# Performance work log

Hardware: AMD Instinct MI355X
Metric: run time of the kernel (lower is better)

## Reference

```python
import jax, jax.numpy as jnp
import numpy as np

B, O, R = 4, 1000, 20000
NF, RD, ED = 6, 1, 100
RH, OH = 150, 100


def setup_inputs() -> dict:
    key = jax.random.key(0)
    ks = jax.random.split(key, 20)
    s = 0.05
    inp = {
        "objects": jax.random.normal(ks[0], (B, O, NF), jnp.float32),
        "sender_relations": jax.random.uniform(ks[1], (B, O, R), jnp.float32),
        "receiver_relations": jax.random.uniform(ks[2], (B, O, R), jnp.float32),
        "relation_info": jax.random.normal(ks[3], (B, R, RD), jnp.float32),
        # relational MLP: (2*NF+RD) -> 150 -> 150 -> 150 -> ED, ReLU after every layer
        "rw1": jax.random.normal(ks[4], (2 * NF + RD, RH), jnp.float32) * s,
        "rb1": jnp.zeros((RH,), jnp.float32),
        "rw2": jax.random.normal(ks[5], (RH, RH), jnp.float32) * s,
        "rb2": jnp.zeros((RH,), jnp.float32),
        "rw3": jax.random.normal(ks[6], (RH, RH), jnp.float32) * s,
        "rb3": jnp.zeros((RH,), jnp.float32),
        "rw4": jax.random.normal(ks[7], (RH, ED), jnp.float32) * s,
        "rb4": jnp.zeros((ED,), jnp.float32),
        # object MLP: (NF+ED) -> 100 -> 2, ReLU only after first layer
        "ow1": jax.random.normal(ks[8], (NF + ED, OH), jnp.float32) * s,
        "ob1": jnp.zeros((OH,), jnp.float32),
        "ow2": jax.random.normal(ks[9], (OH, 2), jnp.float32) * s,
        "ob2": jnp.zeros((2,), jnp.float32),
    }
    return inp


def reference(objects, sender_relations, receiver_relations, relation_info,
              rw1, rb1, rw2, rb2, rw3, rb3, rw4, rb4,
              ow1, ob1, ow2, ob2):
    # marshalling: dense one-hot gather via bmm
    senders = jnp.einsum('bnr,bnf->brf', sender_relations, objects)    # [B,R,NF]
    receivers = jnp.einsum('bnr,bnf->brf', receiver_relations, objects)  # [B,R,NF]
    Bm = jnp.concatenate([senders, receivers, relation_info], axis=2)  # [B,R,2NF+RD]
    # relational MLP (ReLU after every layer, including the last)
    h = jax.nn.relu(Bm @ rw1 + rb1)
    h = jax.nn.relu(h @ rw2 + rb2)
    h = jax.nn.relu(h @ rw3 + rb3)
    E = jax.nn.relu(h @ rw4 + rb4)                                     # [B,R,ED]
    # aggregator: dense scatter via bmm
    effect_receivers = jnp.einsum('bnr,brf->bnf', receiver_relations, E)  # [B,O,ED]
    C = jnp.concatenate([objects, effect_receivers], axis=2)           # [B,O,NF+ED]
    # object MLP, flattened over batch*objects like the torch view(-1, input)
    Cf = C.reshape(-1, C.shape[-1])
    o = jax.nn.relu(Cf @ ow1 + ob1)
    return o @ ow2 + ob2                                               # [B*O, 2]
```

## Files before the change

kernel.cpp:

```cpp
#include <hip/hip_runtime.h>

#define B_   4
#define O_   1000
#define R_   20000
#define NF_  6
#define EDP_ 128
#define KS_  25
#define CHUNK_ 800
#define MPAD_ 1024

#define ET_OFF   5120000
#define PART_OFF 10240000
#define SLAB_    1280000
#define WT_USHORTS (4 * 2 * 25600)

typedef short bf16x8 __attribute__((ext_vector_type(8)));
typedef float f32x4  __attribute__((ext_vector_type(4)));
typedef unsigned short ushort4v __attribute__((ext_vector_type(4)));
typedef unsigned short ushort8v __attribute__((ext_vector_type(8)));

#define MFMA16 __builtin_amdgcn_mfma_f32_16x16x32_bf16

__device__ __forceinline__ unsigned short f2bf(float x) {
    union { float f; unsigned int u; } v; v.f = x;
    unsigned int r = (v.u + 0x7FFFu + ((v.u >> 16) & 1u)) >> 16;
    return (unsigned short)r;
}

__device__ __forceinline__ float bf2f(unsigned short h) {
    union { unsigned int u; float f; } v; v.u = (unsigned int)h << 16;
    return v.f;
}

__global__ __launch_bounds__(256) void k_prep(
    const float* __restrict__ rw1, const float* __restrict__ rb1,
    const float* __restrict__ rw2, const float* __restrict__ rb2,
    const float* __restrict__ rw3, const float* __restrict__ rb3,
    const float* __restrict__ rw4, const float* __restrict__ rb4,
    unsigned short* __restrict__ Wt, float* __restrict__ bfp)
{
    const int l = blockIdx.y;
    const float* Ws[4] = {rw1, rw2, rw3, rw4};
    const float* Bs[4] = {rb1, rb2, rb3, rb4};
    const int   Ksz[4] = {13, 150, 150, 150};
    const int   Nsz[4] = {150, 150, 150, 100};
    const float* w = Ws[l];
    const int K = Ksz[l], N = Nsz[l];

    int idx = blockIdx.x * 256 + threadIdx.x;
    if (idx < 25600) {
        int n = idx / 160, k = idx % 160;
        float v = (k < K && n < N) ? w[k * N + n] : 0.f;
        unsigned short h = f2bf(v);
        unsigned short lo = f2bf(v - bf2f(h));
        Wt[(size_t)l * 51200 + idx]         = h;
        Wt[(size_t)l * 51200 + 25600 + idx] = lo;
    }
    if (blockIdx.x == 0 && threadIdx.x < 160)
        bfp[l * 160 + threadIdx.x] = (threadIdx.x < (unsigned)N) ? Bs[l][threadIdx.x] : 0.f;
}

__global__ __launch_bounds__(256) void k_marshal(
    const float* __restrict__ obj, const float* __restrict__ S,
    const float* __restrict__ RRm, const float* __restrict__ rinfo,
    float* __restrict__ bmp)
{
    __shared__ float sobj[250 * NF_];
    const int b = blockIdx.y, z = blockIdx.z;
    const int n0 = z * 250;
    for (int i = threadIdx.x; i < 250 * NF_; i += 256)
        sobj[i] = obj[(size_t)b * O_ * NF_ + (size_t)n0 * NF_ + i];
    __syncthreads();

    const int r = blockIdx.x * 256 + threadIdx.x;
    if (r >= R_) return;

    const size_t base = (size_t)b * O_ * R_ + (size_t)n0 * R_ + r;
    const float* Sp = S + base;
    const float* Rp = RRm + base;

    float ss[NF_] = {0.f, 0.f, 0.f, 0.f, 0.f, 0.f};
    float rs[NF_] = {0.f, 0.f, 0.f, 0.f, 0.f, 0.f};

    #pragma unroll 4
    for (int n = 0; n < 250; ++n) {
        float sv = Sp[(size_t)n * R_];
        float rv = Rp[(size_t)n * R_];
        #pragma unroll
        for (int f = 0; f < NF_; ++f) {
            float o = sobj[n * NF_ + f];
            ss[f] = fmaf(sv, o, ss[f]);
            rs[f] = fmaf(rv, o, rs[f]);
        }
    }

    float* outp = bmp + (size_t)z * SLAB_ + ((size_t)b * R_ + r) * 16;
    #pragma unroll
    for (int f = 0; f < NF_; ++f) {
        outp[f]     = ss[f];
        outp[6 + f] = rs[f];
    }
    outp[12] = (z == 0) ? rinfo[(size_t)b * R_ + r] : 0.f;
}

template<int NT>
__device__ __forceinline__ void layer_mm(
    const unsigned short (*act)[168],
    const unsigned short* __restrict__ Wh, const unsigned short* __restrict__ Wl,
    int arow, int koff, int cl, f32x4* acc)
{
    #pragma unroll
    for (int n = 0; n < NT; ++n) acc[n] = (f32x4){0.f, 0.f, 0.f, 0.f};
    #pragma unroll
    for (int ks = 0; ks < 5; ++ks) {
        bf16x8 a = *(const bf16x8*)&act[arow][ks * 32 + koff];
        #pragma unroll
        for (int n = 0; n < NT; ++n) {
            bf16x8 wh = *(const bf16x8*)(Wh + (size_t)(n * 16 + cl) * 160 + ks * 32 + koff);
            bf16x8 wl = *(const bf16x8*)(Wl + (size_t)(n * 16 + cl) * 160 + ks * 32 + koff);
            acc[n] = MFMA16(a, wh, acc[n], 0, 0, 0);
            acc[n] = MFMA16(a, wl, acc[n], 0, 0, 0);
        }
    }
}

template<int NT>
__device__ __forceinline__ void epi(
    f32x4* acc, const float* __restrict__ bias,
    unsigned short (*out)[168], int m0, int cl, int rg0)
{
    __syncthreads();
    #pragma unroll
    for (int n = 0; n < NT; ++n) {
        int col = n * 16 + cl;
        float bv = bias[col];
        #pragma unroll
        for (int rg = 0; rg < 4; ++rg) {
            float v = fmaxf(acc[n][rg] + bv, 0.f);
            out[m0 + rg0 + rg][col] = f2bf(v);
        }
    }
    __syncthreads();
}

__global__ __launch_bounds__(256) void k_mlp(
    const float* __restrict__ bmp, unsigned short* __restrict__ Et,
    const unsigned short* __restrict__ Wt, const float* __restrict__ bfp)
{
    __shared__ unsigned short act[64][168];
    __shared__ unsigned short alo[64][32];
    const int t = threadIdx.x;
    const size_t row0 = (size_t)blockIdx.x * 64;

    for (int idx = t; idx < 64 * 32; idx += 256) {
        int rr = idx >> 5, k = idx & 31;
        float v = 0.f;
        if (k < 13) {
            size_t e = (row0 + rr) * 16 + k;
            v = bmp[e] + bmp[(size_t)SLAB_ + e]
              + bmp[2 * (size_t)SLAB_ + e] + bmp[3 * (size_t)SLAB_ + e];
        }
        unsigned short h = f2bf(v);
        act[rr][k] = h;
        alo[rr][k] = f2bf(v - bf2f(h));
    }
    __syncthreads();

    const int lane = t & 63, wave = t >> 6;
    const int m0   = wave * 16;
    const int arow = m0 + (lane & 15);
    const int koff = (lane >> 4) * 8;
    const int cl   = lane & 15;
    const int rg0  = (lane >> 4) * 4;

    f32x4 acc[10];

    {
        const unsigned short* Wh = Wt;
        const unsigned short* Wl = Wt + 25600;
        bf16x8 ah = *(const bf16x8*)&act[arow][koff];
        bf16x8 al = *(const bf16x8*)&alo[arow][koff];
        #pragma unroll
        for (int n = 0; n < 10; ++n) {
            bf16x8 wh = *(const bf16x8*)(Wh + (size_t)(n * 16 + cl) * 160 + koff);
            bf16x8 wl = *(const bf16x8*)(Wl + (size_t)(n * 16 + cl) * 160 + koff);
            f32x4 a = (f32x4){0.f, 0.f, 0.f, 0.f};
            a = MFMA16(ah, wh, a, 0, 0, 0);
            a = MFMA16(ah, wl, a, 0, 0, 0);
            a = MFMA16(al, wh, a, 0, 0, 0);
            acc[n] = a;
        }
    }
    epi<10>(acc, bfp + 0 * 160, act, m0, cl, rg0);

    layer_mm<10>(act, Wt + 1 * 51200, Wt + 1 * 51200 + 25600, arow, koff, cl, acc);
    epi<10>(acc, bfp + 1 * 160, act, m0, cl, rg0);

    layer_mm<10>(act, Wt + 2 * 51200, Wt + 2 * 51200 + 25600, arow, koff, cl, acc);
    epi<10>(acc, bfp + 2 * 160, act, m0, cl, rg0);

    layer_mm<7>(act, Wt + 3 * 51200, Wt + 3 * 51200 + 25600, arow, koff, cl, acc);
    epi<7>(acc, bfp + 3 * 160, act, m0, cl, rg0);

    for (int idx = t; idx < 64 * 128; idx += 256) {
        int rr = idx & 63, j = idx >> 6;
        size_t gr = row0 + rr;
        int b = (int)(gr / R_);
        int r = (int)(gr - (size_t)b * R_);
        Et[((size_t)(b * EDP_ + j)) * R_ + r] = (j < 100) ? act[rr][j] : (unsigned short)0;
    }
}

__global__ __launch_bounds__(256) void k_agg(
    const float* __restrict__ RRm, const unsigned short* __restrict__ Et,
    float* __restrict__ part)
{
    __shared__ unsigned short sB[2][128][36];
    const int t = threadIdx.x;
    const int mt = blockIdx.x, b = blockIdx.y, kz = blockIdx.z;
    const int lane = t & 63, wave = t >> 6;
    const int k0 = kz * CHUNK_;

    const int br0 = t >> 2, bc0 = (t & 3) * 8;
    const int br1 = br0 + 64;
    const unsigned short* EtB = Et + (size_t)b * EDP_ * R_;

    const int cl = lane & 15, koff = (lane >> 4) * 8;
    int n0 = mt * 128 + wave * 32 + cl;
    int n1 = n0 + 16;
    if (n0 > 999) n0 = 999;
    if (n1 > 999) n1 = 999;
    const float* Ap0 = RRm + ((size_t)(b * O_) + n0) * R_ + k0 + koff;
    const float* Ap1 = RRm + ((size_t)(b * O_) + n1) * R_ + k0 + koff;

    f32x4 acc[2][8] = {};
    float4 a0c, a1c, a2c, a3c;
    float4 a0n = {0,0,0,0}, a1n = {0,0,0,0}, a2n = {0,0,0,0}, a3n = {0,0,0,0};

    {
        ushort8v v0 = *(const ushort8v*)(EtB + (size_t)br0 * R_ + k0 + bc0);
        ushort8v v1 = *(const ushort8v*)(EtB + (size_t)br1 * R_ + k0 + bc0);
        *(ushort8v*)&sB[0][br0][bc0] = v0;
        *(ushort8v*)&sB[0][br1][bc0] = v1;
        a0c = *(const float4*)(Ap0 + 0);
        a1c = *(const float4*)(Ap0 + 4);
        a2c = *(const float4*)(Ap1 + 0);
        a3c = *(const float4*)(Ap1 + 4);
    }
    __syncthreads();

    for (int it = 0; it < CHUNK_ / 32; ++it) {
        const int cur = it & 1, nxt = cur ^ 1;
        const bool more = (it + 1 < CHUNK_ / 32);
        ushort8v v0, v1;
        if (more) {
            const int kb = k0 + (it + 1) * 32;
            v0 = *(const ushort8v*)(EtB + (size_t)br0 * R_ + kb + bc0);
            v1 = *(const ushort8v*)(EtB + (size_t)br1 * R_ + kb + bc0);
            a0n = *(const float4*)(Ap0 + (it + 1) * 32);
            a1n = *(const float4*)(Ap0 + (it + 1) * 32 + 4);
            a2n = *(const float4*)(Ap1 + (it + 1) * 32);
            a3n = *(const float4*)(Ap1 + (it + 1) * 32 + 4);
        }
        bf16x8 af0, af1;
        af0[0] = (short)f2bf(a0c.x); af0[1] = (short)f2bf(a0c.y);
        af0[2] = (short)f2bf(a0c.z); af0[3] = (short)f2bf(a0c.w);
        af0[4] = (short)f2bf(a1c.x); af0[5] = (short)f2bf(a1c.y);
        af0[6] = (short)f2bf(a1c.z); af0[7] = (short)f2bf(a1c.w);
        af1[0] = (short)f2bf(a2c.x); af1[1] = (short)f2bf(a2c.y);
        af1[2] = (short)f2bf(a2c.z); af1[3] = (short)f2bf(a2c.w);
        af1[4] = (short)f2bf(a3c.x); af1[5] = (short)f2bf(a3c.y);
        af1[6] = (short)f2bf(a3c.z); af1[7] = (short)f2bf(a3c.w);
        #pragma unroll
        for (int ni = 0; ni < 8; ++ni) {
            bf16x8 bf = *(const bf16x8*)&sB[cur][ni * 16 + cl][koff];
            acc[0][ni] = MFMA16(af0, bf, acc[0][ni], 0, 0, 0);
            acc[1][ni] = MFMA16(af1, bf, acc[1][ni], 0, 0, 0);
        }
        if (more) {
            *(ushort8v*)&sB[nxt][br0][bc0] = v0;
            *(ushort8v*)&sB[nxt][br1][bc0] = v1;
        }
        __syncthreads();
        a0c = a0n; a1c = a1n; a2c = a2n; a3c = a3n;
    }

    float* pp = part + ((size_t)(kz * 4 + b) * MPAD_) * 128;
    #pragma unroll
    for (int mg = 0; mg < 2; ++mg) {
        const int rowb = mt * 128 + wave * 32 + mg * 16 + (lane >> 4) * 4;
        #pragma unroll
        for (int ni = 0; ni < 8; ++ni)
            #pragma unroll
            for (int rg = 0; rg < 4; ++rg)
                pp[(size_t)(rowb + rg) * 128 + ni * 16 + cl] = acc[mg][ni][rg];
    }
}

__global__ __launch_bounds__(256) void k_obj(
    const float* __restrict__ obj, const float* __restrict__ part,
    const float* __restrict__ ow1, const float* __restrict__ ob1,
    const float* __restrict__ ow2, const float* __restrict__ ob2,
    float* __restrict__ out)
{
    __shared__ float C[8][112];
    __shared__ float h[8][104];
    const int t = threadIdx.x;
    const int g0 = blockIdx.x * 8;

    for (int idx = t; idx < 8 * NF_; idx += 256) {
        int rr = idx / NF_, f = idx % NF_;
        C[rr][f] = obj[(size_t)(g0 + rr) * NF_ + f];
    }
    for (int idx = t; idx < 8 * 100; idx += 256) {
        int rr = idx / 100, f = idx % 100;
        int g = g0 + rr, b = g / 1000, n = g % 1000;
        float s = 0.f;
        for (int z = 0; z < KS_; ++z)
            s += part[((size_t)(z * 4 + b) * MPAD_ + n) * 128 + f];
        C[rr][6 + f] = s;
    }
    __syncthreads();

    for (int idx = t; idx < 8 * 100; idx += 256) {
        int rr = idx / 100, j = idx % 100;
        float acc = ob1[j];
        for (int k = 0; k < 106; ++k)
            acc = fmaf(C[rr][k], ow1[k * 100 + j], acc);
        h[rr][j] = fmaxf(acc, 0.f);
    }
    __syncthreads();

    if (t < 16) {
        int rr = t >> 1, j = t & 1;
        float acc = ob2[j];
        for (int k = 0; k < 100; ++k)
            acc = fmaf(h[rr][k], ow2[k * 2 + j], acc);
        out[(size_t)(g0 + rr) * 2 + j] = acc;
    }
}

extern "C" void kernel_launch(void* const* d_in, const int* in_sizes, int n_in,
                              void* d_out, int out_size, void* d_ws, size_t ws_size,
                              hipStream_t stream)
{
    const float* obj   = (const float*)d_in[0];
    const float* S     = (const float*)d_in[1];
    const float* RRm   = (const float*)d_in[2];
    const float* rinfo = (const float*)d_in[3];
    const float* rw1   = (const float*)d_in[4];
    const float* rb1   = (const float*)d_in[5];
    const float* rw2   = (const float*)d_in[6];
    const float* rb2   = (const float*)d_in[7];
    const float* rw3   = (const float*)d_in[8];
    const float* rb3   = (const float*)d_in[9];
    const float* rw4   = (const float*)d_in[10];
    const float* rb4   = (const float*)d_in[11];
    const float* ow1   = (const float*)d_in[12];
    const float* ob1   = (const float*)d_in[13];
    const float* ow2   = (const float*)d_in[14];
    const float* ob2   = (const float*)d_in[15];

    float* ws            = (float*)d_ws;
    float* bmp           = ws;
    unsigned short* Et   = (unsigned short*)(ws + ET_OFF);
    float* part          = ws + PART_OFF;
    unsigned short* Wt   = (unsigned short*)(ws + PART_OFF);
    float* bfp           = ws + PART_OFF + (WT_USHORTS / 2);
    float* out           = (float*)d_out;

    k_prep<<<dim3(100, 4), 256, 0, stream>>>(rw1, rb1, rw2, rb2, rw3, rb3, rw4, rb4,
                                             Wt, bfp);
    k_marshal<<<dim3(79, 4, 4), 256, 0, stream>>>(obj, S, RRm, rinfo, bmp);
    k_mlp<<<dim3(1250), 256, 0, stream>>>(bmp, Et, Wt, bfp);
    k_agg<<<dim3(8, 4, KS_), 256, 0, stream>>>(RRm, Et, part);
    k_obj<<<dim3(500), 256, 0, stream>>>(obj, part, ow1, ob1, ow2, ob2, out);
}
```

Measured before the change: 384.1 us.

## Stage marshal relation tiles via direct global-to-LDS loads with finer split-K

The marshal kernel now splits the object dimension into 10 slabs of 100 instead of 4 of 250, which gives more blocks to stream the two large relation matrices. Tiles of 10 rows are copied from global memory straight into LDS with the async global_load_lds instruction, then consumed from shared memory between barriers. Output rows are written as four float4 stores, and the last block is clamped so it recomputes an overlapping range instead of masking threads. The cost is that the MLP kernel must now sum 10 partial slabs, which adds workspace traffic and needs a larger workspace.

```diff
diff --git a/kernel.cpp b/kernel.cpp
--- a/kernel.cpp
+++ b/kernel.cpp
@@ -9,9 +9,10 @@
 #define CHUNK_ 800
 #define MPAD_ 1024
 
-#define ET_OFF   5120000
-#define PART_OFF 10240000
 #define SLAB_    1280000
+#define NSLAB_   10
+#define ET_OFF   12800000
+#define PART_OFF 17920000
 #define WT_USHORTS (4 * 2 * 25600)
 
 typedef short bf16x8 __attribute__((ext_vector_type(8)));
@@ -60,47 +61,69 @@
         bfp[l * 160 + threadIdx.x] = (threadIdx.x < (unsigned)N) ? Bs[l][threadIdx.x] : 0.f;
 }
 
+#define NTILE_ 10
 __global__ __launch_bounds__(256) void k_marshal(
     const float* __restrict__ obj, const float* __restrict__ S,
     const float* __restrict__ RRm, const float* __restrict__ rinfo,
     float* __restrict__ bmp)
 {
-    __shared__ float sobj[250 * NF_];
+    __shared__ float sS[NTILE_][256];
+    __shared__ float sR[NTILE_][256];
+    __shared__ float sobj[100 * NF_];
+    const int t = threadIdx.x;
     const int b = blockIdx.y, z = blockIdx.z;
-    const int n0 = z * 250;
-    for (int i = threadIdx.x; i < 250 * NF_; i += 256)
+    const int n0 = z * 100;
+    int r0 = blockIdx.x * 256;
+    if (r0 > R_ - 256) r0 = R_ - 256;
+
+    for (int i = t; i < 100 * NF_; i += 256)
         sobj[i] = obj[(size_t)b * O_ * NF_ + (size_t)n0 * NF_ + i];
-    __syncthreads();
-
-    const int r = blockIdx.x * 256 + threadIdx.x;
-    if (r >= R_) return;
-
-    const size_t base = (size_t)b * O_ * R_ + (size_t)n0 * R_ + r;
+
+    const int wave = t >> 6, lane = t & 63;
+    const size_t base = (size_t)b * O_ * R_ + (size_t)n0 * R_ + r0;
     const float* Sp = S + base;
     const float* Rp = RRm + base;
 
     float ss[NF_] = {0.f, 0.f, 0.f, 0.f, 0.f, 0.f};
     float rs[NF_] = {0.f, 0.f, 0.f, 0.f, 0.f, 0.f};
 
-    #pragma unroll 4
-    for (int n = 0; n < 250; ++n) {
-        float sv = Sp[(size_t)n * R_];
-        float rv = Rp[(size_t)n * R_];
-        #pragma unroll
-        for (int f = 0; f < NF_; ++f) {
-            float o = sobj[n * NF_ + f];
-            ss[f] = fmaf(sv, o, ss[f]);
-            rs[f] = fmaf(rv, o, rs[f]);
-        }
-    }
-
-    float* outp = bmp + (size_t)z * SLAB_ + ((size_t)b * R_ + r) * 16;
-    #pragma unroll
-    for (int f = 0; f < NF_; ++f) {
-        outp[f]     = ss[f];
-        outp[6 + f] = rs[f];
-    }
-    outp[12] = (z == 0) ? rinfo[(size_t)b * R_ + r] : 0.f;
+    for (int tile = 0; tile < 100 / NTILE_; ++tile) {
+        const int nb = tile * NTILE_;
+        for (int p = wave; p < 2 * NTILE_; p += 4) {
+            const int n = p >> 1;
+            const float* gsrc = ((p & 1) ? Rp : Sp) + (size_t)(nb + n) * R_ + lane * 4;
+            float* ldst = (p & 1) ? &sR[n][0] : &sS[n][0];
+            __builtin_amdgcn_global_load_lds(
+                (const __attribute__((address_space(1))) void*)gsrc,
+                (__attribute__((address_space(3))) void*)ldst, 16, 0, 0);
+        }
+        __syncthreads();
+        #pragma unroll
+        for (int n = 0; n < NTILE_; ++n) {
+            float sv = sS[n][t];
+            float rv = sR[n][t];
+            const float* o = &sobj[(nb + n) * NF_];
+            #pragma unroll
+            for (int f = 0; f < NF_; ++f) {
+                float ov = o[f];
+                ss[f] = fmaf(sv, ov, ss[f]);
+                rs[f] = fmaf(rv, ov, rs[f]);
+            }
+        }
+        __syncthreads();
+    }
+
+    float riv = 0.f;
+    if (z == 0) riv = rinfo[(size_t)b * R_ + r0 + t];
+    float* outp = bmp + (size_t)z * SLAB_ + ((size_t)b * R_ + r0 + t) * 16;
+    float4 w0 = {ss[0], ss[1], ss[2], ss[3]};
+    float4 w1 = {ss[4], ss[5], rs[0], rs[1]};
+    float4 w2 = {rs[2], rs[3], rs[4], rs[5]};
+    float4 w3 = {riv, 0.f, 0.f, 0.f};
+    *(float4*)(outp + 0)  = w0;
+    *(float4*)(outp + 4)  = w1;
+    *(float4*)(outp + 8)  = w2;
+    *(float4*)(outp + 12) = w3;
 }
 
 template<int NT>
@@ -157,8 +180,9 @@
         float v = 0.f;
         if (k < 13) {
             size_t e = (row0 + rr) * 16 + k;
-            v = bmp[e] + bmp[(size_t)SLAB_ + e]
-              + bmp[2 * (size_t)SLAB_ + e] + bmp[3 * (size_t)SLAB_ + e];
+            #pragma unroll
+            for (int s = 0; s < NSLAB_; ++s)
+                v += bmp[(size_t)s * SLAB_ + e];
         }
         unsigned short h = f2bf(v);
         act[rr][k] = h;
@@ -371,7 +395,7 @@
 
     k_prep<<<dim3(100, 4), 256, 0, stream>>>(rw1, rb1, rw2, rb2, rw3, rb3, rw4, rb4,
                                              Wt, bfp);
-    k_marshal<<<dim3(79, 4, 4), 256, 0, stream>>>(obj, S, RRm, rinfo, bmp);
+    k_marshal<<<dim3(79, 4, 10), 256, 0, stream>>>(obj, S, RRm, rinfo, bmp);
     k_mlp<<<dim3(1250), 256, 0, stream>>>(bmp, Et, Wt, bfp);
     k_agg<<<dim3(8, 4, KS_), 256, 0, stream>>>(RRm, Et, part);
     k_obj<<<dim3(500), 256, 0, stream>>>(obj, part, ow1, ob1, ow2, ob2, out);
```

Result: slower. 397.1 us (+3.4%).
